# Kernel tuning notes

Hardware: AMD Instinct MI355X
Metric: run time of the kernel (lower is better)

## Reference

```python
import jax, jax.numpy as jnp
import numpy as np


def reference(x, phi, sigma, M_phi_plus, M_phi_minus, M_u, padded_sl):
    """STU forward: spectral FFT convolution + autoregressive input term.

    x:   (B, L, D) input sequence
    phi: (L, K) time-domain spectral filters (top-K Hankel eigenvectors);
         V = rfft(phi, n=padded_sl) matches the module's precomputed V.
    sigma: (K,) Hankel eigenvalues
    M_phi_plus/minus: (K, D, D) per-filter projections
    M_u: (k_u, D, D) AR-on-input matrices
    """
    B, L, D = x.shape
    K = sigma.shape[0]
    n = padded_sl  # FFT length for causal linear convolution

    # Alternating-sign trick for the 'minus' featurization:
    # sum_j (-1)^j phi_j u_{t-j} = (-1)^t * conv(phi, sgn*u)_t
    sgn = jnp.where(jnp.arange(L) % 2 == 0, 1.0, -1.0).astype(x.dtype)[None, :, None]  # (1,L,1)

    V = jnp.fft.rfft(phi, n=n, axis=0)                       # (n//2+1, K) complex
    U = jnp.fft.rfft(jnp.stack([x, x * sgn], axis=-1), n=n, axis=1)  # (B, n//2+1, D, 2)
    prod = V[None, :, :, None, None] * U[:, :, None, :, :]    # (B, n//2+1, K, D, 2)
    conv = jnp.fft.irfft(prod, n=n, axis=1)[:, :L]            # (B, L, K, D, 2) causal conv
    U_plus = conv[..., 0]
    U_minus = conv[..., 1] * sgn[..., None]                   # undo sign on output side

    # Fold sigma^{1/4} scaling into the projection matrices.
    sig4 = (sigma ** 0.25).astype(x.dtype)[:, None, None]     # (K,1,1)
    spectral = (
        jnp.einsum('blkd,kdo->blo', U_plus, M_phi_plus * sig4)
        + jnp.einsum('blkd,kdo->blo', U_minus, M_phi_minus * sig4)
    )

    # compute_ar_u: y_t += sum_{i=0}^{k_u-1} x_{t-i} @ M_u[i]  (use_ar_u=True)
    ar_u = jnp.einsum('bld,do->blo', x, M_u[0])
    for i in range(1, M_u.shape[0]):  # small fixed depth k_u=3
        x_shift = jnp.pad(x, ((0, 0), (i, 0), (0, 0)))[:, :L]
        ar_u = ar_u + jnp.einsum('bld,do->blo', x_shift, M_u[i])

    # use_ar_y=False branch; dropout=0 (identity)
    return spectral + ar_u


def setup_inputs() -> dict:
    key = jax.random.key(0)
    ks = jax.random.split(key, 6)
    B, L, D, K, KU, N = 1, 2048, 768, 16, 3, 4096
    x = jax.random.normal(ks[0], (B, L, D), jnp.float32)
    phi = jax.random.normal(ks[1], (L, K), jnp.float32) / np.sqrt(L).astype(np.float32)
    sigma = jax.random.uniform(ks[2], (K,), jnp.float32, 0.1, 1.0)
    M_phi_plus = jax.random.normal(ks[3], (K, D, D), jnp.float32) * 0.02
    M_phi_minus = jax.random.normal(ks[4], (K, D, D), jnp.float32) * 0.02
    M_u = jax.random.normal(ks[5], (KU, D, D), jnp.float32) * 0.02
    return {"x": x, "phi": phi, "sigma": sigma, "M_phi_plus": M_phi_plus,
            "M_phi_minus": M_phi_minus, "M_u": M_u, "padded_sl": N}
```

## Files before the change

kernel.cpp:

```cpp
#include <hip/hip_runtime.h>

typedef __attribute__((ext_vector_type(8))) short bf16x8;
typedef __attribute__((ext_vector_type(8))) short short8;
typedef __attribute__((ext_vector_type(4))) short short4v;
typedef __attribute__((ext_vector_type(4))) float f32x4;

#define SL 2048
#define DM 768
#define NCH 32
#define MSPEC 24576
#define MTOT  26880

#define SPLITK 10
#define KSLICE 2688
#define NT2 42
#define NITER2 21

#define WS_U      0ULL
#define WS_TMAT   110100480ULL
#define WS_XT     126910464ULL
#define WS_MCAT   130056192ULL
#define WS_PART   171343872ULL
#define WS_NEED   234258432ULL

#define NB_M   5040
#define NB_T   4104
#define NB_AR  768
#define NB_XT  384
#define NB_ALL (NB_M + NB_T + NB_AR + NB_XT)

__device__ __forceinline__ short f2bf(float f) {
  unsigned u = __builtin_bit_cast(unsigned, f);
  u = (u + 0x7FFFu + ((u >> 16) & 1u)) >> 16;
  return (short)u;
}

__device__ __forceinline__ void gload16(const short* g, short* l) {
  __builtin_amdgcn_global_load_lds(
      (const __attribute__((address_space(1))) void*)g,
      (__attribute__((address_space(3))) void*)l, 16, 0, 0);
}


__global__ __launch_bounds__(256) void k_zero(float4* out) {
  out[blockIdx.x * 256 + threadIdx.x] = float4{0.f, 0.f, 0.f, 0.f};
}

__global__ __launch_bounds__(256) void k_prep_all(const float* __restrict__ x,
                                                  const float* __restrict__ phi,
                                                  const float* __restrict__ sigma,
                                                  const float* __restrict__ Mp,
                                                  const float* __restrict__ Mm,
                                                  const float* __restrict__ Mu,
                                                  short* __restrict__ xT,
                                                  short* __restrict__ U,
                                                  short* __restrict__ Tmat,
                                                  short* __restrict__ McatT) {
  __shared__ short tile[64][65];
  const int b = blockIdx.x;
  const int t = threadIdx.x;

  if (b < NB_M) {
    __shared__ float s4l[16];
    if (t < 16) s4l[t] = sqrtf(sqrtf(sigma[t]));
    __syncthreads();
    const int m0 = (b % 420) * 64, o0 = (b / 420) * 64;
#pragma unroll
    for (int rr = 0; rr < 16; ++rr) {
      int ml = rr * 4 + (t >> 6), ol = t & 63;
      int m = m0 + ml, o = o0 + ol;
      float v;
      if (m < MSPEC) {
        int c = m / DM, d = m - c * DM;
        float s4 = s4l[c & 15];
        if (c < 16) v = Mp[((size_t)c * DM + d) * DM + o] * s4;
        else        v = Mm[((size_t)(c - 16) * DM + d) * DM + o] * s4;
      } else {
        int mm = m - MSPEC;
        int i = mm / DM, d = mm - i * DM;
        v = Mu[((size_t)i * DM + d) * DM + o];
      }
      tile[ml][ol] = f2bf(v);
    }
    __syncthreads();
#pragma unroll
    for (int i = 0; i < 4; ++i) {
      int u = i * 256 + t;
      int ol = u >> 4, ml0 = (u & 15) * 4;
      short4v v = {tile[ml0][ol], tile[ml0 + 1][ol],
                   tile[ml0 + 2][ol], tile[ml0 + 3][ol]};
      *reinterpret_cast<short4v*>(&McatT[(size_t)(o0 + ol) * MTOT + m0 + ml0]) = v;
    }
    return;
  }
  if (b < NB_M + NB_T) {
    int idx = ((b - NB_M) * 256 + t) * 8;
    int c = idx >> 18;
    short8 v = {0, 0, 0, 0, 0, 0, 0, 0};
    if (c < 32) {
      int b0 = idx & 127, a = (idx >> 7) & 127, dlag = (idx >> 14) & 15;
      int j0 = dlag * 128 + a - b0;
#pragma unroll
      for (int e = 0; e < 8; ++e) {
        int j = j0 - e;
        if (j >= 0) {
          float p = phi[j * 16 + (c & 15)];
          if (c >= 16 && (j & 1)) p = -p;
          v[e] = f2bf(p);
        }
      }
    }
    *reinterpret_cast<short8*>(&Tmat[idx]) = v;
    return;
  }
  if (b < NB_M + NB_T + NB_AR) {
    int tid = (b - NB_M - NB_T) * 256 + t;
    int l = tid / 96, d0 = (tid - l * 96) * 8;
#pragma unroll
    for (int i = 0; i < 3; ++i) {
      short8 v = {0, 0, 0, 0, 0, 0, 0, 0};
      if (l >= i) {
        const float* src = &x[(size_t)(l - i) * DM + d0];
#pragma unroll
        for (int e = 0; e < 8; ++e) v[e] = f2bf(src[e]);
      }
      *reinterpret_cast<short8*>(&U[(size_t)l * MTOT + MSPEC + i * DM + d0]) = v;
    }
    return;
  }
  {
    const int bb = b - NB_M - NB_T - NB_AR;
    const int d0 = (bb % 12) * 64, l0 = (bb / 12) * 64;
#pragma unroll
    for (int rr = 0; rr < 16; ++rr) {
      int ll = rr * 4 + (t >> 6), dl = t & 63;
      tile[ll][dl] = f2bf(x[(size_t)(l0 + ll) * DM + d0 + dl]);
    }
    __syncthreads();
#pragma unroll
    for (int rr = 0; rr < 16; ++rr) {
      int dl = rr * 4 + (t >> 6), ll = t & 63;
      xT[(size_t)(d0 + dl) * SL + l0 + ll] = tile[ll][dl];
    }
  }
}


#define LDSREADS(BUF, KS, MQ)                                                   \
    _Pragma("unroll")                                                           \
    for (int q_ = 0; q_ < 4; ++q_)                                              \
      af_[q_] = *reinterpret_cast<const bf16x8*>(                               \
          &As[BUF][KS][wm1][((MQ) * 64 + q_ * 16 + lrow) * 32 + foff]);         \
    if ((MQ) == 0) {                                                            \
      _Pragma("unroll")                                                         \
      for (int i_ = 0; i_ < 4; ++i_)                                            \
        bf_[i_] = *reinterpret_cast<const bf16x8*>(                             \
            &Bs[BUF][KS][hB][(rB0 + i_ * 16 + lrow) * 32 + foff]);              \
    }

#define DOMFMA(MQ)                                                              \
    _Pragma("unroll")                                                           \
    for (int q_ = 0; q_ < 4; ++q_)                                              \
      _Pragma("unroll")                                                         \
      for (int i_ = 0; i_ < 4; ++i_)                                            \
        acc[(MQ) * 4 + q_][i_] = __builtin_amdgcn_mfma_f32_16x16x32_bf16(       \
            af_[q_], bf_[i_], acc[(MQ) * 4 + q_][i_], 0, 0, 0)

#define PHASE(BUF, KS, MQ, VMODE, STG) do {                                     \
    bf16x8 af_[4];                                                              \
    if ((VMODE) == 1) asm volatile("s_waitcnt vmcnt(6)" ::: "memory");          \
    if ((VMODE) == 2) {                                                         \
      if (j < nIterM1) asm volatile("s_waitcnt vmcnt(6)" ::: "memory");         \
      else             asm volatile("s_waitcnt vmcnt(0)" ::: "memory");         \
    }                                                                           \
    if ((VMODE) == 0) { LDSREADS(BUF, KS, MQ) }                                 \
    STG;                                                                        \
    if ((VMODE) != 0) {                                                         \
      __builtin_amdgcn_s_barrier();                                             \
      asm volatile("" ::: "memory");                                            \
      LDSREADS(BUF, KS, MQ)                                                     \
    }                                                                           \
    __builtin_amdgcn_s_setprio(1);                                              \
    DOMFMA(MQ);                                                                 \
    __builtin_amdgcn_s_setprio(0);                                              \
    asm volatile("s_waitcnt lgkmcnt(0)" ::: "memory");                          \
    __builtin_amdgcn_s_barrier();                                               \
  } while (0)


#define STA1(SBUF, SKS, SKT) do { int kt_ = (SKT); if (kt_ < nT) {              \
    int kch_ = kt_ * 64 + (SKS) * 32;                                           \
    int kb_ = kch_ >> 7, bo_ = kch_ & 127;                                      \
    int dl_ = 2 * rt - kb_;                                                     \
    const short* g0_ = (dl_ >= 0) ? (Tc + ((size_t)dl_ << 14) + bo_)            \
                                  : (Tz + bo_);                                 \
    const short* g1_ = Tc + ((size_t)(dl_ + 1) << 14) + bo_;                    \
    gload16(g0_, &As[SBUF][SKS][0][t8]);                                        \
    gload16(g1_, &As[SBUF][SKS][1][t8]); } } while (0)

#define STB1(SBUF, SKS, SKT) do { int kt_ = (SKT); if (kt_ < nT) {              \
    const short* g_ = Bb + kt_ * 64 + (SKS) * 32;                               \
    gload16(g_, &Bs[SBUF][SKS][0][t8]);                                         \
    gload16(g_ + (size_t)128 * SL, &Bs[SBUF][SKS][1][t8]); } } while (0)

__global__ __launch_bounds__(512, 2) void k_gemm1_8p(const short* __restrict__ Tmat,
                                                     const short* __restrict__ xT,
                                                     short* __restrict__ U) {
  __shared__ __align__(16) short As[2][2][2][4096];
  __shared__ __align__(16) short Bs[2][2][2][4096];
  const int bid = blockIdx.x;
  const int xcd = bid & 7;
  const int slot = bid >> 3;
  const int c = xcd * 4 + (slot & 3);
  const int q = slot >> 2;
  const int ct = q % 3;
  const int rt = 7 - q / 3;
  const int nT = 4 * (rt + 1);
  const int nIter = 2 * (rt + 1);
  const int nIterM1 = nIter - 1;
  const int t = threadIdx.x;
  const int lane = t & 63, wave = t >> 6;
  const int wm1 = wave >> 2;
  const int hB = (wave & 3) >> 1;
  const int rB0 = (wave & 1) * 64;
  const int lrow = lane & 15, quad = lane >> 4;
  const int foff = (quad ^ ((lrow >> 1) & 3)) << 3;
  const int r = t >> 2;
  const int cswz = ((t & 3) ^ ((r >> 1) & 3)) << 3;
  const int t8 = t * 8;

  const short* Tc = Tmat + ((size_t)(c * 16) << 14) + r * 128 + cswz;
  const short* Tz = Tmat + ((size_t)512 << 14) + r * 128 + cswz;
  const short* Bb = xT + (size_t)(ct * 256 + r) * SL + cswz;

  f32x4 acc[8][4] = {};

  STB1(0, 0, 0); STA1(0, 0, 0); STB1(0, 1, 0); STA1(0, 1, 0);
  STB1(1, 0, 1); STA1(1, 0, 1); STB1(1, 1, 1);

  for (int j = 0; j < nIter; ++j) {
    bf16x8 bf_[4];
    PHASE(0, 0, 0, 1, STA1(1, 1, 2 * j + 1));
    PHASE(0, 0, 1, 0, STB1(0, 0, 2 * j + 2));
    PHASE(0, 1, 0, 0, STA1(0, 0, 2 * j + 2));
    PHASE(0, 1, 1, 0, STB1(0, 1, 2 * j + 2));
    PHASE(1, 0, 0, 2, STA1(0, 1, 2 * j + 2));
    PHASE(1, 0, 1, 0, STB1(1, 0, 2 * j + 3));
    PHASE(1, 1, 0, 0, STA1(1, 0, 2 * j + 3));
    PHASE(1, 1, 1, 0, STB1(1, 1, 2 * j + 3));
  }

  const int wm128 = (wave >> 2) * 128, wn64 = (wave & 3) * 64;
  const int l0 = rt * 256, colbase = c * DM + ct * 256;
#pragma unroll
  for (int im = 0; im < 8; ++im)
#pragma unroll
    for (int in = 0; in < 4; ++in)
#pragma unroll
      for (int r4 = 0; r4 < 4; ++r4) {
        int row = l0 + wm128 + im * 16 + quad * 4 + r4;
        int col = colbase + wn64 + in * 16 + lrow;
        U[(size_t)row * MTOT + col] = f2bf(acc[im][in][r4]);
      }
}


#define STA2(SBUF, SKS, SKT) do { int kt_ = (SKT); if (kt_ < NT2) {             \
    const short* g_ = Abase + kt_ * 64 + (SKS) * 32;                            \
    gload16(g_, &As[SBUF][SKS][0][t8]);                                         \
    gload16(g_ + (size_t)128 * MTOT, &As[SBUF][SKS][1][t8]); } } while (0)

#define STB2(SBUF, SKS, SKT) do { int kt_ = (SKT); if (kt_ < NT2) {             \
    const short* g_ = Bbase + kt_ * 64 + (SKS) * 32;                            \
    gload16(g_, &Bs[SBUF][SKS][0][t8]);                                         \
    gload16(g_ + (size_t)128 * MTOT, &Bs[SBUF][SKS][1][t8]); } } while (0)

__global__ __launch_bounds__(512, 2) void k_gemm2_8p(const short* __restrict__ U,
                                                     const short* __restrict__ McatT,
                                                     float* __restrict__ out,
                                                     float* __restrict__ part,
                                                     int use_part) {
  __shared__ __align__(16) short As[2][2][2][4096];
  __shared__ __align__(16) short Bs[2][2][2][4096];
  const int bid = blockIdx.x;
  const int tile = bid % 24, kc = bid / 24;
  const int mt = tile & 7, nt_ = tile >> 3;
  const int m0 = mt * 256, o0 = nt_ * 256;
  const int kbase = kc * KSLICE;
  const int t = threadIdx.x;
  const int lane = t & 63, wave = t >> 6;
  const int wm1 = wave >> 2;
  const int hB = (wave & 3) >> 1;
  const int rB0 = (wave & 1) * 64;
  const int lrow = lane & 15, quad = lane >> 4;
  const int foff = (quad ^ ((lrow >> 1) & 3)) << 3;
  const int r = t >> 2;
  const int cswz = ((t & 3) ^ ((r >> 1) & 3)) << 3;
  const int t8 = t * 8;
  const int nIterM1 = NITER2 - 1;

  const short* Abase = U     + (size_t)(m0 + r) * MTOT + kbase + cswz;
  const short* Bbase = McatT + (size_t)(o0 + r) * MTOT + kbase + cswz;

  f32x4 acc[8][4] = {};

  STB2(0, 0, 0); STA2(0, 0, 0); STB2(0, 1, 0); STA2(0, 1, 0);
  STB2(1, 0, 1); STA2(1, 0, 1); STB2(1, 1, 1);

  for (int j = 0; j < NITER2; ++j) {
    bf16x8 bf_[4];
    PHASE(0, 0, 0, 1, STA2(1, 1, 2 * j + 1));
    PHASE(0, 0, 1, 0, STB2(0, 0, 2 * j + 2));
    PHASE(0, 1, 0, 0, STA2(0, 0, 2 * j + 2));
    PHASE(0, 1, 1, 0, STB2(0, 1, 2 * j + 2));
    PHASE(1, 0, 0, 2, STA2(0, 1, 2 * j + 2));
    PHASE(1, 0, 1, 0, STB2(1, 0, 2 * j + 3));
    PHASE(1, 1, 0, 0, STA2(1, 0, 2 * j + 3));
    PHASE(1, 1, 1, 0, STB2(1, 1, 2 * j + 3));
  }

  const int wm128 = (wave >> 2) * 128, wn64 = (wave & 3) * 64;
  if (use_part) {
    float* dst = part + (size_t)kc * (2048 * 768);
#pragma unroll
    for (int im = 0; im < 8; ++im)
#pragma unroll
      for (int in = 0; in < 4; ++in)
#pragma unroll
        for (int r4 = 0; r4 < 4; ++r4) {
          int row = m0 + wm128 + im * 16 + quad * 4 + r4;
          int col = o0 + wn64 + in * 16 + lrow;
          dst[(size_t)row * DM + col] = acc[im][in][r4];
        }
  } else {
#pragma unroll
    for (int im = 0; im < 8; ++im)
#pragma unroll
      for (int in = 0; in < 4; ++in)
#pragma unroll
        for (int r4 = 0; r4 < 4; ++r4) {
          int row = m0 + wm128 + im * 16 + quad * 4 + r4;
          int col = o0 + wn64 + in * 16 + lrow;
          atomicAdd(&out[(size_t)row * DM + col], acc[im][in][r4]);
        }
  }
}

__global__ __launch_bounds__(256) void k_reduce(const float4* __restrict__ part,
                                                float4* __restrict__ out) {
  int i = blockIdx.x * 256 + threadIdx.x;
  float4 s = part[i];
#pragma unroll
  for (int k = 1; k < SPLITK; ++k) {
    float4 v = part[(size_t)k * 393216 + i];
    s.x += v.x; s.y += v.y; s.z += v.z; s.w += v.w;
  }
  out[i] = s;
}

extern "C" void kernel_launch(void* const* d_in, const int* in_sizes, int n_in,
                              void* d_out, int out_size, void* d_ws, size_t ws_size,
                              hipStream_t stream) {
  (void)in_sizes; (void)n_in; (void)out_size;
  const float* x     = (const float*)d_in[0];
  const float* phi   = (const float*)d_in[1];
  const float* sigma = (const float*)d_in[2];
  const float* Mp    = (const float*)d_in[3];
  const float* Mm    = (const float*)d_in[4];
  const float* Mu    = (const float*)d_in[5];
  float* out = (float*)d_out;
  char* ws = (char*)d_ws;

  short* U     = (short*)(ws + WS_U);
  short* Tmat  = (short*)(ws + WS_TMAT);
  short* xT    = (short*)(ws + WS_XT);
  short* McatT = (short*)(ws + WS_MCAT);
  float* Wpart = (float*)(ws + WS_PART);
  const int use_part = ws_size >= WS_NEED ? 1 : 0;

  if (!use_part)
    k_zero<<<dim3(1536), dim3(256), 0, stream>>>((float4*)out);
  k_prep_all<<<dim3(NB_ALL), dim3(256), 0, stream>>>(x, phi, sigma, Mp, Mm, Mu,
                                                     xT, U, Tmat, McatT);
  k_gemm1_8p<<<dim3(768), dim3(512), 0, stream>>>(Tmat, xT, U);
  k_gemm2_8p<<<dim3(240), dim3(512), 0, stream>>>(U, McatT, out, Wpart, use_part);
  if (use_part)
    k_reduce<<<dim3(1536), dim3(256), 0, stream>>>((const float4*)Wpart, (float4*)out);
}
```

Baseline: 356.4 us.

## Split prep kernel and overlap weight conversion with first GEMM

The single prep kernel is split in two. Only the Toeplitz matrix and the transposed x, which GEMM1 consumes, are built before GEMM1. The conversion of the projection weights to bf16 and the AR input-shift columns are moved into extra blocks appended to the GEMM1 grid, each 512-thread block handling two 256-thread prep tiles and reusing the GEMM shared memory. This lets the bandwidth-heavy weight transpose run alongside GEMM1 compute instead of serially before it. The cost is contention for CU slots and memory bandwidth with GEMM1 blocks, plus __syncthreads inside a half-block branch, which is safe only because both halves take the same path in every block except possibly the last.

```diff
diff --git a/kernel.cpp b/kernel.cpp
--- a/kernel.cpp
+++ b/kernel.cpp
@@ -27,7 +27,7 @@
 #define NB_T   4104
 #define NB_AR  768
 #define NB_XT  384
-#define NB_ALL (NB_M + NB_T + NB_AR + NB_XT)
+#define NPREP2 ((NB_M + NB_AR) / 2)
 
 __device__ __forceinline__ short f2bf(float f) {
   unsigned u = __builtin_bit_cast(unsigned, f);
@@ -46,55 +46,16 @@
   out[blockIdx.x * 256 + threadIdx.x] = float4{0.f, 0.f, 0.f, 0.f};
 }
 
-__global__ __launch_bounds__(256) void k_prep_all(const float* __restrict__ x,
-                                                  const float* __restrict__ phi,
-                                                  const float* __restrict__ sigma,
-                                                  const float* __restrict__ Mp,
-                                                  const float* __restrict__ Mm,
-                                                  const float* __restrict__ Mu,
-                                                  short* __restrict__ xT,
-                                                  short* __restrict__ U,
-                                                  short* __restrict__ Tmat,
-                                                  short* __restrict__ McatT) {
+__global__ __launch_bounds__(256) void k_prep_g1(const float* __restrict__ x,
+                                                 const float* __restrict__ phi,
+                                                 short* __restrict__ xT,
+                                                 short* __restrict__ Tmat) {
   __shared__ short tile[64][65];
   const int b = blockIdx.x;
   const int t = threadIdx.x;
 
-  if (b < NB_M) {
-    __shared__ float s4l[16];
-    if (t < 16) s4l[t] = sqrtf(sqrtf(sigma[t]));
-    __syncthreads();
-    const int m0 = (b % 420) * 64, o0 = (b / 420) * 64;
-#pragma unroll
-    for (int rr = 0; rr < 16; ++rr) {
-      int ml = rr * 4 + (t >> 6), ol = t & 63;
-      int m = m0 + ml, o = o0 + ol;
-      float v;
-      if (m < MSPEC) {
-        int c = m / DM, d = m - c * DM;
-        float s4 = s4l[c & 15];
-        if (c < 16) v = Mp[((size_t)c * DM + d) * DM + o] * s4;
-        else        v = Mm[((size_t)(c - 16) * DM + d) * DM + o] * s4;
-      } else {
-        int mm = m - MSPEC;
-        int i = mm / DM, d = mm - i * DM;
-        v = Mu[((size_t)i * DM + d) * DM + o];
-      }
-      tile[ml][ol] = f2bf(v);
-    }
-    __syncthreads();
-#pragma unroll
-    for (int i = 0; i < 4; ++i) {
-      int u = i * 256 + t;
-      int ol = u >> 4, ml0 = (u & 15) * 4;
-      short4v v = {tile[ml0][ol], tile[ml0 + 1][ol],
-                   tile[ml0 + 2][ol], tile[ml0 + 3][ol]};
-      *reinterpret_cast<short4v*>(&McatT[(size_t)(o0 + ol) * MTOT + m0 + ml0]) = v;
-    }
-    return;
-  }
-  if (b < NB_M + NB_T) {
-    int idx = ((b - NB_M) * 256 + t) * 8;
+  if (b < NB_T) {
+    int idx = (b * 256 + t) * 8;
     int c = idx >> 18;
     short8 v = {0, 0, 0, 0, 0, 0, 0, 0};
     if (c < 32) {
@@ -113,23 +74,8 @@
     *reinterpret_cast<short8*>(&Tmat[idx]) = v;
     return;
   }
-  if (b < NB_M + NB_T + NB_AR) {
-    int tid = (b - NB_M - NB_T) * 256 + t;
-    int l = tid / 96, d0 = (tid - l * 96) * 8;
-#pragma unroll
-    for (int i = 0; i < 3; ++i) {
-      short8 v = {0, 0, 0, 0, 0, 0, 0, 0};
-      if (l >= i) {
-        const float* src = &x[(size_t)(l - i) * DM + d0];
-#pragma unroll
-        for (int e = 0; e < 8; ++e) v[e] = f2bf(src[e]);
-      }
-      *reinterpret_cast<short8*>(&U[(size_t)l * MTOT + MSPEC + i * DM + d0]) = v;
-    }
-    return;
-  }
   {
-    const int bb = b - NB_M - NB_T - NB_AR;
+    const int bb = b - NB_T;
     const int d0 = (bb % 12) * 64, l0 = (bb / 12) * 64;
 #pragma unroll
     for (int rr = 0; rr < 16; ++rr) {
@@ -203,12 +149,76 @@
     gload16(g_, &Bs[SBUF][SKS][0][t8]);                                         \
     gload16(g_ + (size_t)128 * SL, &Bs[SBUF][SKS][1][t8]); } } while (0)
 
-__global__ __launch_bounds__(512, 2) void k_gemm1_8p(const short* __restrict__ Tmat,
-                                                     const short* __restrict__ xT,
-                                                     short* __restrict__ U) {
+__global__ __launch_bounds__(512, 2) void k_gemm1p(const short* __restrict__ Tmat,
+                                                   const short* __restrict__ xT,
+                                                   short* __restrict__ U,
+                                                   const float* __restrict__ sigma,
+                                                   const float* __restrict__ Mp,
+                                                   const float* __restrict__ Mm,
+                                                   const float* __restrict__ Mu,
+                                                   const float* __restrict__ x,
+                                                   short* __restrict__ McatT) {
   __shared__ __align__(16) short As[2][2][2][4096];
   __shared__ __align__(16) short Bs[2][2][2][4096];
   const int bid = blockIdx.x;
+  const int t = threadIdx.x;
+
+  if (bid >= 768) {
+    const int p = bid - 768;
+    const int half = t >> 8;
+    const int tt = t & 255;
+    const int ob = 2 * p + half;
+    short* tbase = &As[0][0][0][0] + half * 4608;
+    short (*tl)[65] = reinterpret_cast<short(*)[65]>(tbase);
+    float* s4l = reinterpret_cast<float*>(&Bs[0][0][0][0]) + half * 16;
+
+    if (ob < NB_M) {
+      if (tt < 16) s4l[tt] = sqrtf(sqrtf(sigma[tt]));
+      __syncthreads();
+      const int m0 = (ob % 420) * 64, o0 = (ob / 420) * 64;
+#pragma unroll
+      for (int rr = 0; rr < 16; ++rr) {
+        int ml = rr * 4 + (tt >> 6), ol = tt & 63;
+        int m = m0 + ml, o = o0 + ol;
+        float v;
+        if (m < MSPEC) {
+          int c = m / DM, d = m - c * DM;
+          float s4 = s4l[c & 15];
+          if (c < 16) v = Mp[((size_t)c * DM + d) * DM + o] * s4;
+          else        v = Mm[((size_t)(c - 16) * DM + d) * DM + o] * s4;
+        } else {
+          int mm = m - MSPEC;
+          int i = mm / DM, d = mm - i * DM;
+          v = Mu[((size_t)i * DM + d) * DM + o];
+        }
+        tl[ml][ol] = f2bf(v);
+      }
+      __syncthreads();
+#pragma unroll
+      for (int i = 0; i < 4; ++i) {
+        int u = i * 256 + tt;
+        int ol = u >> 4, ml0 = (u & 15) * 4;
+        short4v v = {tl[ml0][ol], tl[ml0 + 1][ol],
+                     tl[ml0 + 2][ol], tl[ml0 + 3][ol]};
+        *reinterpret_cast<short4v*>(&McatT[(size_t)(o0 + ol) * MTOT + m0 + ml0]) = v;
+      }
+    } else {
+      int tid = (ob - NB_M) * 256 + tt;
+      int l = tid / 96, d0 = (tid - l * 96) * 8;
+#pragma unroll
+      for (int i = 0; i < 3; ++i) {
+        short8 v = {0, 0, 0, 0, 0, 0, 0, 0};
+        if (l >= i) {
+          const float* src = &x[(size_t)(l - i) * DM + d0];
+#pragma unroll
+          for (int e = 0; e < 8; ++e) v[e] = f2bf(src[e]);
+        }
+        *reinterpret_cast<short8*>(&U[(size_t)l * MTOT + MSPEC + i * DM + d0]) = v;
+      }
+    }
+    return;
+  }
+
   const int xcd = bid & 7;
   const int slot = bid >> 3;
   const int c = xcd * 4 + (slot & 3);
@@ -218,7 +228,6 @@
   const int nT = 4 * (rt + 1);
   const int nIter = 2 * (rt + 1);
   const int nIterM1 = nIter - 1;
-  const int t = threadIdx.x;
   const int lane = t & 63, wave = t >> 6;
   const int wm1 = wave >> 2;
   const int hB = (wave & 3) >> 1;
@@ -380,9 +389,9 @@
 
   if (!use_part)
     k_zero<<<dim3(1536), dim3(256), 0, stream>>>((float4*)out);
-  k_prep_all<<<dim3(NB_ALL), dim3(256), 0, stream>>>(x, phi, sigma, Mp, Mm, Mu,
-                                                     xT, U, Tmat, McatT);
-  k_gemm1_8p<<<dim3(768), dim3(512), 0, stream>>>(Tmat, xT, U);
+  k_prep_g1<<<dim3(NB_T + NB_XT), dim3(256), 0, stream>>>(x, phi, xT, Tmat);
+  k_gemm1p<<<dim3(768 + NPREP2), dim3(512), 0, stream>>>(Tmat, xT, U, sigma,
+                                                         Mp, Mm, Mu, x, McatT);
   k_gemm2_8p<<<dim3(240), dim3(512), 0, stream>>>(U, McatT, out, Wpart, use_part);
   if (use_part)
     k_reduce<<<dim3(1536), dim3(256), 0, stream>>>((const float4*)Wpart, (float4*)out);
```

After: 436.6 us. +22.5%, slower.
